# Performance work log

Measured on AMD Instinct MI355X. Metric: run time of the kernel, lower is better.

## Reference

```python
import jax, jax.numpy as jnp
import numpy as np

RES, SKIP, NCLS, K = 256, 512, 256, 2
NUM_LAYERS, NUM_STACKS = 10, 3
NL = NUM_LAYERS * NUM_STACKS
DILATIONS = [2 ** (i % NUM_LAYERS) for i in range(NL)]


def _causal_conv(x, W, b, dilation):
    # x: [B, Cin, T], W: [Cout, Cin, K] -> [B, Cout, T]
    # Original pads both sides by d*(K-1) then slices the right pad off,
    # which is exactly a left-only pad.
    pad = dilation * (W.shape[-1] - 1)
    y = jax.lax.conv_general_dilated(
        x, W, window_strides=(1,), padding=[(pad, 0)],
        rhs_dilation=(dilation,), dimension_numbers=('NCH', 'OIH', 'NCH'))
    return y + b[None, :, None]


def _pw(x, W, b):
    # 1x1 conv: x [B,C,T], W [O,C] -> [B,O,T]
    return jnp.einsum('oc,bct->bot', W, x) + b[None, :, None]


def setup_inputs() -> dict:
    key = jax.random.key(0)
    ks = jax.random.split(key, 16)
    s = 0.05
    return {
        'x': jax.random.normal(ks[0], (4, 1, 8192), dtype=jnp.float32),
        'W_start': jax.random.normal(ks[1], (RES, 1, K), dtype=jnp.float32) * s,
        'b_start': jnp.zeros((RES,), dtype=jnp.float32),
        'Wd': jax.random.normal(ks[2], (NL, RES, RES, K), dtype=jnp.float32) * s,
        'bd': jnp.zeros((NL, RES), dtype=jnp.float32),
        'Wr': jax.random.normal(ks[3], (NL, RES, RES), dtype=jnp.float32) * s,
        'br': jnp.zeros((NL, RES), dtype=jnp.float32),
        'Ws': jax.random.normal(ks[4], (NL, SKIP, RES), dtype=jnp.float32) * s,
        'bs': jnp.zeros((NL, SKIP), dtype=jnp.float32),
        'W_end1': jax.random.normal(ks[5], (SKIP, SKIP), dtype=jnp.float32) * s,
        'b_end1': jnp.zeros((SKIP,), dtype=jnp.float32),
        'W_end2': jax.random.normal(ks[6], (NCLS, SKIP), dtype=jnp.float32) * s,
        'b_end2': jnp.zeros((NCLS,), dtype=jnp.float32),
    }


def reference(x, W_start, b_start, Wd, bd, Wr, br, Ws, bs, W_end1, b_end1, W_end2, b_end2):
    h = _causal_conv(x, W_start, b_start, 1)  # [B, RES, T]
    skip_sum = jnp.zeros((x.shape[0], SKIP, x.shape[2]), dtype=x.dtype)
    for i in range(NL):
        d = _causal_conv(h, Wd[i], bd[i], DILATIONS[i])
        gated = jnp.tanh(d) * jax.nn.sigmoid(d)
        h = h + _pw(gated, Wr[i], br[i])
        skip_sum = skip_sum + _pw(gated, Ws[i], bs[i])
    out = jax.nn.relu(skip_sum)
    out = jax.nn.relu(_pw(out, W_end1, b_end1))
    out = _pw(out, W_end2, b_end2)
    return out[:, :, -1]  # [B, NCLS]
```

## Files before the change

### kernel.cpp

```cpp
#include <hip/hip_runtime.h>

#define BATCH 4
#define T 8192
#define RES 256
#define SKIPC 512
#define NCLSC 256
#define NLAYERS 30
#define T0 5120
#define TBUF 3072
#define NT 32
#define STR 264
#define HFSTR 260
#define GRIDP 384
#define MAXTILES 96

typedef __attribute__((ext_vector_type(8))) short short8x;
typedef __attribute__((ext_vector_type(4))) float floatx4;
typedef unsigned short ushort_t;
typedef unsigned long long ull;

__device__ __forceinline__ ushort_t f2bf(float f) {
    unsigned u = __float_as_uint(f);
    u += 0x7fffu + ((u >> 16) & 1u);
    return (ushort_t)(u >> 16);
}
__device__ __forceinline__ float bf2f(ushort_t h) {
    return __uint_as_float(((unsigned)h) << 16);
}

__device__ __forceinline__ ull cload(const ull* p) {
    return __hip_atomic_load(p, __ATOMIC_RELAXED, __HIP_MEMORY_SCOPE_AGENT);
}
__device__ __forceinline__ void cstore(ull* p, ull v) {
    __hip_atomic_store(p, v, __ATOMIC_RELAXED, __HIP_MEMORY_SCOPE_AGENT);
}

#define WAITF(P) while (__hip_atomic_load((P), __ATOMIC_RELAXED, __HIP_MEMORY_SCOPE_AGENT) == 0) \
                     __builtin_amdgcn_s_sleep(1)

#define MFMA __builtin_amdgcn_mfma_f32_16x16x32_bf16

__global__ __launch_bounds__(256) void prep_kernel(
    const float* __restrict__ Wd, const float* __restrict__ Wr,
    const float* __restrict__ Ws,
    ushort_t* __restrict__ Aswz, ushort_t* __restrict__ Rswz,
    ushort_t* __restrict__ WsT)
{
    long id = (long)blockIdx.x * 256 + threadIdx.x;
    const long R0 = 30L * 131072, R1 = 30L * 65536, R2 = 30L * 131072;
    if (id < R0) {
        long l = id >> 17; int r = (int)(id & 131071);
        int j = r & 7, lane = (r >> 3) & 63, f = (r >> 9) & 1, s = (r >> 10) & 15, wv = r >> 14;
        int row = wv * 32 + f * 16 + (lane & 15);
        int k = s * 32 + (lane >> 4) * 8 + j;
        int cin = k & 255, kk = k >> 8;
        Aswz[id] = f2bf(Wd[((l * 256 + row) * 256 + cin) * 2 + kk]);
        return;
    }
    id -= R0;
    if (id < R1) {
        long l = id >> 16; int r = (int)(id & 65535);
        int j = r & 7, lane = (r >> 3) & 63, f = (r >> 9) & 1, s = (r >> 10) & 7, wv = r >> 13;
        int row = wv * 32 + f * 16 + (lane & 15);
        int k = s * 32 + (lane >> 4) * 8 + j;
        Rswz[id] = f2bf(Wr[(l * 256 + row) * 256 + k]);
        return;
    }
    id -= R1;
    if (id < R2) {
        int o = (int)(id & 511); long rest = id >> 9; int cin = (int)(rest & 255); long l = rest >> 8;
        WsT[id] = f2bf(Ws[(l * 512 + o) * 256 + cin]);
    }
}

__global__ __launch_bounds__(256) void start_kernel(
    const float* __restrict__ x, const float* __restrict__ Wst,
    const float* __restrict__ bst, float* __restrict__ hf, ushort_t* __restrict__ hb)
{
    int id = blockIdx.x * 256 + threadIdx.x;
    int c = id & 255;
    int ti = (id >> 8) % TBUF;
    int b  = (id >> 8) / TBUF;
    int t = T0 + ti;
    float v = Wst[2 * c] * x[b * T + t - 1] + Wst[2 * c + 1] * x[b * T + t] + bst[c];
    hf[id] = v;
    hb[id] = f2bf(v);
}

__global__ __launch_bounds__(512, 2) void fused_layers_kernel(
    const float* __restrict__ hf,
    const ushort_t* __restrict__ hb0,
    const ushort_t* __restrict__ Asw,
    const float* __restrict__ bd,
    const ushort_t* __restrict__ Rsw,
    const float* __restrict__ br,
    float* __restrict__ gstore,
    ushort_t* __restrict__ hbC,
    int* __restrict__ flg)
{
    __shared__ __align__(16) ushort_t hbL[NT * STR];
    __shared__ __align__(16) ushort_t tp[NT * STR];
    __shared__ __align__(16) float hfL[NT * HFSTR];

    const int tid = threadIdx.x;
    const int wv = tid >> 6, lane = tid & 63;
    const int quad = lane >> 4, l16 = lane & 15;
    const int mb = wv * 32;
    const int u0 = l16 * STR + quad * 8;
    const int u1 = u0 + 16 * STR;
    const int B = blockIdx.x;
    const int b = B / MAXTILES, tile = B % MAXTILES;
    const int tb = 8192 - NT * (tile + 1);

    const float* __restrict__ hfg = hf + (size_t)b * TBUF * RES;
    const ushort_t* __restrict__ hbg = hb0 + (size_t)b * TBUF * RES;

    #pragma unroll
    for (int p = 0; p < 4; ++p) {
        int c = p * 512 + tid;
        int row = c >> 6, q = (c & 63) * 4;
        *(float4*)&hfL[row * HFSTR + q] =
            *(const float4*)(hfg + (size_t)(tb - T0 + row) * RES + q);
    }
    #pragma unroll
    for (int p = 0; p < 2; ++p) {
        int c = p * 512 + tid;
        int row = c >> 5, q = (c & 31) * 8;
        *(short8x*)&hbL[row * STR + q] =
            *(const short8x*)(hbg + (size_t)(tb - T0 + row) * RES + q);
    }
    __syncthreads();

    int rem = 3069;
    int ntiles_prev = 0;
    size_t cur_off = 0, prev_off = 0;

    for (int i = 0; i < NLAYERS; ++i) {
        const int dil = 1 << (i % 10);
        rem -= dil;
        const int s_out = 8191 - rem;
        const int ntiles = (1 + rem + 31) >> 5;
        if (tile >= ntiles) break;

        const ushort_t* __restrict__ aw =
            Asw + (size_t)i * (RES * 512) + (size_t)wv * 16384 + lane * 8;
        const ushort_t* __restrict__ rw =
            Rsw + (size_t)i * (RES * RES) + (size_t)wv * 8192 + lane * 8;
        const float* __restrict__ bdL = bd + i * RES;
        const float* __restrict__ brL = br + i * RES;

        const int dil_eff = dil < NT ? dil : NT;
        const int rdelta = dil < NT ? 1 : (dil >> 5);
        const int r = tile + rdelta;
        const bool remote_valid = (i > 0) && (r < ntiles_prev);
        const bool do_stage = (i == 0) || remote_valid;
        const ushort_t* hbCp = nullptr;
        if (remote_valid)
            hbCp = hbC + prev_off + ((size_t)b * ntiles_prev + r) * (size_t)dil_eff * RES;

        const ushort_t* bp0 = ((l16      >= dil_eff) ? &hbL[(l16      - dil) * STR]
                                                     : &tp[l16 * STR]) + quad * 8;
        const ushort_t* bp1 = ((16 + l16 >= dil_eff) ? &hbL[(16 + l16 - dil) * STR]
                                                     : &tp[(16 + l16) * STR]) + quad * 8;

        floatx4 acc00, acc01, acc10, acc11;
        {
            float4 c0 = *(const float4*)(bdL + mb + quad * 4);
            float4 c1 = *(const float4*)(bdL + mb + 16 + quad * 4);
            acc00 = acc01 = (floatx4){c0.x, c0.y, c0.z, c0.w};
            acc10 = acc11 = (floatx4){c1.x, c1.y, c1.z, c1.w};
        }

        #define LD(BASE, S, OFF) (*(const short8x*)((BASE) + (S) * 1024 + (OFF)))

        {
            short8x a0 = LD(aw, 8, 0), a1 = LD(aw, 8, 512);
            #pragma unroll
            for (int s = 0; s < 8; ++s) {
                short8x n0 = a0, n1 = a1;
                if (s < 7) { n0 = LD(aw, 9 + s, 0); n1 = LD(aw, 9 + s, 512); }
                const int ko = s * 32;
                short8x g0 = *(const short8x*)&hbL[ko + u0];
                short8x g1 = *(const short8x*)&hbL[ko + u1];
                acc00 = MFMA(a0, g0, acc00, 0, 0, 0);
                acc10 = MFMA(a1, g0, acc10, 0, 0, 0);
                acc01 = MFMA(a0, g1, acc01, 0, 0, 0);
                acc11 = MFMA(a1, g1, acc11, 0, 0, 0);
                a0 = n0; a1 = n1;
            }
        }

        if (do_stage) {
            if (i > 0) { WAITF(flg + ((i - 1) * BATCH + b) * MAXTILES + r); }
            if (i == 0) {
                #pragma unroll
                for (int p = 0; p < 2; ++p) {
                    int c = p * 512 + tid;
                    int row = c >> 5, q = (c & 31) * 8;
                    if (row < dil_eff) {
                        int tt = tb + row - dil;
                        tt = tt < T0 ? T0 : tt;
                        *(short8x*)&tp[row * STR + q] =
                            *(const short8x*)(hbg + (size_t)(tt - T0) * RES + q);
                    }
                }
            } else {
                #pragma unroll
                for (int p = 0; p < 2; ++p) {
                    int c = p * 512 + tid;
                    int row = c >> 5, q = (c & 31) * 8;
                    if (row < dil_eff) {
                        const ull* src = (const ull*)(hbCp + (size_t)row * RES + q);
                        ull v0 = cload(src), v1 = cload(src + 1);
                        ull* dst = (ull*)&tp[row * STR + q];
                        dst[0] = v0; dst[1] = v1;
                    }
                }
            }
            __syncthreads();
        }

        {
            short8x a0 = LD(aw, 0, 0), a1 = LD(aw, 0, 512);
            #pragma unroll
            for (int s = 0; s < 8; ++s) {
                short8x n0 = a0, n1 = a1;
                if (s < 7) { n0 = LD(aw, 1 + s, 0); n1 = LD(aw, 1 + s, 512); }
                const int ko = s * 32;
                short8x g0 = *(const short8x*)(bp0 + ko);
                short8x g1 = *(const short8x*)(bp1 + ko);
                acc00 = MFMA(a0, g0, acc00, 0, 0, 0);
                acc10 = MFMA(a1, g0, acc10, 0, 0, 0);
                acc01 = MFMA(a0, g1, acc01, 0, 0, 0);
                acc11 = MFMA(a1, g1, acc11, 0, 0, 0);
                a0 = n0; a1 = n1;
            }
        }

        short8x ra0 = LD(rw, 0, 0), ra1 = LD(rw, 0, 512);
        __syncthreads();

        #define GATE(ACC, MF, NF) do {                                             \
            float gf[4]; ull pk = 0;                                               \
            _Pragma("unroll")                                                      \
            for (int rr = 0; rr < 4; ++rr) {                                       \
                float d = fmaxf((ACC)[rr], -30.f);                                 \
                float u = __expf(-d);                                              \
                gf[rr] = (1.f - u) * __builtin_amdgcn_rcpf(1.f + u * u);           \
                pk |= ((ull)f2bf(gf[rr])) << (16 * rr);                            \
            }                                                                      \
            const int n = (NF) * 16 + l16;                                         \
            const int m = mb + (MF) * 16 + quad * 4;                               \
            *(ull*)&tp[n * STR + m] = pk;                                          \
            if (tile == 0 && n == 31) {                                            \
                float4 g4 = {gf[0], gf[1], gf[2], gf[3]};                          \
                *(float4*)&gstore[((size_t)i * BATCH + b) * RES + m] = g4;         \
            }                                                                      \
        } while (0)
        GATE(acc00, 0, 0); GATE(acc01, 0, 1); GATE(acc10, 1, 0); GATE(acc11, 1, 1);
        #undef GATE
        __syncthreads();

        floatx4 r00, r01, r10, r11;
        {
            float4 c0 = *(const float4*)(brL + mb + quad * 4);
            float4 c1 = *(const float4*)(brL + mb + 16 + quad * 4);
            r00 = r01 = (floatx4){c0.x, c0.y, c0.z, c0.w};
            r10 = r11 = (floatx4){c1.x, c1.y, c1.z, c1.w};
        }
        {
            short8x a0 = ra0, a1 = ra1;
            #pragma unroll
            for (int s = 0; s < 8; ++s) {
                short8x n0 = a0, n1 = a1;
                if (s < 7) { n0 = LD(rw, 1 + s, 0); n1 = LD(rw, 1 + s, 512); }
                const int ko = s * 32;
                short8x g0 = *(const short8x*)&tp[ko + u0];
                short8x g1 = *(const short8x*)&tp[ko + u1];
                r00 = MFMA(a0, g0, r00, 0, 0, 0);
                r10 = MFMA(a1, g0, r10, 0, 0, 0);
                r01 = MFMA(a0, g1, r01, 0, 0, 0);
                r11 = MFMA(a1, g1, r11, 0, 0, 0);
                a0 = n0; a1 = n1;
            }
        }
        #undef LD

        const int dnext = (i < NLAYERS - 1) ? (1 << ((i + 1) % 10)) : 0;
        const int Ci = dnext < NT ? dnext : NT;
        const int rdn = (dnext < NT) ? 1 : (dnext >> 5);
        const bool wrC = (Ci > 0) && (tile >= rdn);
        const int pubrow = NT - Ci;
        ushort_t* hbCc = hbC + cur_off + ((size_t)b * ntiles + tile) * (size_t)Ci * RES;

        #define EPI(NF, RA, RB) do {                                               \
            const int n = (NF) * 16 + l16;                                         \
            if (tb + n >= s_out) {                                                 \
                const int m0 = mb + quad * 4;                                      \
                {                                                                  \
                    float4 ho = *(const float4*)&hfL[n * HFSTR + m0];              \
                    float4 hn = {ho.x + (RA)[0], ho.y + (RA)[1],                   \
                                 ho.z + (RA)[2], ho.w + (RA)[3]};                  \
                    *(float4*)&hfL[n * HFSTR + m0] = hn;                           \
                    ull pk = (ull)f2bf(hn.x) | ((ull)f2bf(hn.y) << 16)             \
                           | ((ull)f2bf(hn.z) << 32) | ((ull)f2bf(hn.w) << 48);    \
                    *(ull*)&hbL[n * STR + m0] = pk;                                \
                    if (wrC && n >= pubrow)                                        \
                        cstore((ull*)(hbCc + (size_t)(n - pubrow) * RES + m0), pk);\
                }                                                                  \
                {                                                                  \
                    const int m1 = m0 + 16;                                        \
                    float4 ho = *(const float4*)&hfL[n * HFSTR + m1];              \
                    float4 hn = {ho.x + (RB)[0], ho.y + (RB)[1],                   \
                                 ho.z + (RB)[2], ho.w + (RB)[3]};                  \
                    *(float4*)&hfL[n * HFSTR + m1] = hn;                           \
                    ull pk = (ull)f2bf(hn.x) | ((ull)f2bf(hn.y) << 16)             \
                           | ((ull)f2bf(hn.z) << 32) | ((ull)f2bf(hn.w) << 48);    \
                    *(ull*)&hbL[n * STR + m1] = pk;                                \
                    if (wrC && n >= pubrow)                                        \
                        cstore((ull*)(hbCc + (size_t)(n - pubrow) * RES + m1), pk);\
                }                                                                  \
            }                                                                      \
        } while (0)
        EPI(0, r00, r10);
        EPI(1, r01, r11);
        #undef EPI

        asm volatile("s_waitcnt vmcnt(0)" ::: "memory");
        __syncthreads();
        if (tid == 0)
            __hip_atomic_store(flg + ((size_t)i * BATCH + b) * MAXTILES + tile, 1,
                               __ATOMIC_RELAXED, __HIP_MEMORY_SCOPE_AGENT);

        ntiles_prev = ntiles;
        prev_off = cur_off;
        cur_off += (size_t)BATCH * ntiles * Ci * RES;
    }
}

__global__ __launch_bounds__(512) void skip_kernel(
    const ushort_t* __restrict__ WsT, const float* __restrict__ bs,
    const float* __restrict__ gstore, float* __restrict__ skip)
{
    const int l = blockIdx.x, b = blockIdx.y, o = threadIdx.x;
    const ushort_t* w = WsT + (size_t)l * 131072;
    const float* g = gstore + (size_t)(l * BATCH + b) * RES;
    float a = bs[l * SKIPC + o];
    #pragma unroll 4
    for (int cin = 0; cin < RES; ++cin)
        a = fmaf(bf2f(w[cin * SKIPC + o]), g[cin], a);
    atomicAdd(&skip[b * SKIPC + o], a);
}

__global__ __launch_bounds__(256) void end1_kernel(
    const float* __restrict__ skip, const float* __restrict__ W1,
    const float* __restrict__ b1, float* __restrict__ e1ws)
{
    __shared__ float s[SKIPC];
    __shared__ float part[256];
    const int b = blockIdx.x, og = blockIdx.y, tid = threadIdx.x;
    s[tid]       = fmaxf(skip[b * SKIPC + tid], 0.f);
    s[tid + 256] = fmaxf(skip[b * SKIPC + tid + 256], 0.f);
    __syncthreads();
    const int o_l = tid >> 3, kp = tid & 7;
    const int o = og * 32 + o_l;
    const float* w = W1 + (size_t)o * SKIPC + kp * 64;
    const float* sp = s + kp * 64;
    float a = 0.f;
    #pragma unroll 8
    for (int j = 0; j < 64; ++j) a = fmaf(w[j], sp[j], a);
    part[tid] = a;
    __syncthreads();
    if (tid < 32) {
        float r = b1[og * 32 + tid];
        #pragma unroll
        for (int k = 0; k < 8; ++k) r += part[tid * 8 + k];
        e1ws[b * SKIPC + og * 32 + tid] = fmaxf(r, 0.f);
    }
}

__global__ __launch_bounds__(256) void end2_kernel(
    const float* __restrict__ e1ws, const float* __restrict__ W2,
    const float* __restrict__ b2, float* __restrict__ out)
{
    __shared__ float e[SKIPC];
    __shared__ float part[256];
    const int b = blockIdx.x, og = blockIdx.y, tid = threadIdx.x;
    e[tid]       = e1ws[b * SKIPC + tid];
    e[tid + 256] = e1ws[b * SKIPC + tid + 256];
    __syncthreads();
    const int o_l = tid >> 3, kp = tid & 7;
    const int cls = og * 32 + o_l;
    const float* w = W2 + (size_t)cls * SKIPC + kp * 64;
    const float* ep = e + kp * 64;
    float a = 0.f;
    #pragma unroll 8
    for (int j = 0; j < 64; ++j) a = fmaf(w[j], ep[j], a);
    part[tid] = a;
    __syncthreads();
    if (tid < 32) {
        float r = b2[og * 32 + tid];
        #pragma unroll
        for (int k = 0; k < 8; ++k) r += part[tid * 8 + k];
        out[b * NCLSC + og * 32 + tid] = r;
    }
}

extern "C" void kernel_launch(void* const* d_in, const int* in_sizes, int n_in,
                              void* d_out, int out_size, void* d_ws, size_t ws_size,
                              hipStream_t stream)
{
    const float* x   = (const float*)d_in[0];
    const float* Wst = (const float*)d_in[1];
    const float* bst = (const float*)d_in[2];
    const float* Wd  = (const float*)d_in[3];
    const float* bd  = (const float*)d_in[4];
    const float* Wr  = (const float*)d_in[5];
    const float* br  = (const float*)d_in[6];
    const float* Ws  = (const float*)d_in[7];
    const float* bs  = (const float*)d_in[8];
    const float* W1  = (const float*)d_in[9];
    const float* b1  = (const float*)d_in[10];
    const float* W2  = (const float*)d_in[11];
    const float* b2  = (const float*)d_in[12];
    float* out = (float*)d_out;

    size_t hbC_shorts = 0;
    {
        int rem = 3069;
        for (int i = 0; i < NLAYERS; ++i) {
            int d = 1 << (i % 10);
            rem -= d;
            int ntl = (1 + rem + 31) >> 5;
            int dn = (i < NLAYERS - 1) ? (1 << ((i + 1) % 10)) : 0;
            int Ci = (dn < NT) ? dn : NT;
            hbC_shorts += (size_t)BATCH * ntl * Ci * RES;
        }
    }

    char* w = (char*)d_ws;
    float* hf     = (float*)w;     w += (size_t)BATCH * TBUF * RES * 4;
    ushort_t* hb0 = (ushort_t*)w;  w += (size_t)BATCH * TBUF * RES * 2;
    ushort_t* Asw = (ushort_t*)w;  w += (size_t)NLAYERS * RES * 512 * 2;
    ushort_t* Rsw = (ushort_t*)w;  w += (size_t)NLAYERS * RES * RES * 2;
    ushort_t* WsT = (ushort_t*)w;  w += (size_t)NLAYERS * RES * SKIPC * 2;
    float* gstore = (float*)w;     w += (size_t)NLAYERS * BATCH * RES * 4;
    float* skip   = (float*)w;     w += (size_t)BATCH * SKIPC * 4;
    float* e1ws   = (float*)w;     w += (size_t)BATCH * SKIPC * 4;
    ushort_t* hbC = (ushort_t*)w;  w += hbC_shorts * 2;
    int* flg      = (int*)w;       w += (size_t)NLAYERS * BATCH * MAXTILES * 4;

    prep_kernel<<<38400, 256, 0, stream>>>(Wd, Wr, Ws, Asw, Rsw, WsT);
    start_kernel<<<(BATCH * TBUF * RES) / 256, 256, 0, stream>>>(x, Wst, bst, hf, hb0);
    hipMemsetAsync(skip, 0, BATCH * SKIPC * 4, stream);
    hipMemsetAsync(flg, 0, (size_t)NLAYERS * BATCH * MAXTILES * 4, stream);

    fused_layers_kernel<<<GRIDP, 512, 0, stream>>>(
        hf, hb0, Asw, bd, Rsw, br, gstore, hbC, flg);

    skip_kernel<<<dim3(NLAYERS, BATCH), 512, 0, stream>>>(WsT, bs, gstore, skip);
    end1_kernel<<<dim3(BATCH, 16), 256, 0, stream>>>(skip, W1, b1, e1ws);
    end2_kernel<<<dim3(BATCH, 8), 256, 0, stream>>>(e1ws, W2, b2, out);
}
```

Measured before the change: 420.0 us.

## Vectorize weight prep kernels and software-pipeline MFMA weight loads across phases

Splits the scalar per-element weight conversion kernel into a vectorized Wd/Wr swizzle kernel and a shared-memory transpose kernel for Ws, so prep reads float4 and writes packed 64-bit bf16 groups. In the fused layer kernel, the per-step prefetch loops are replaced by a register double-buffer (q/p banks) with sched barriers. Weight loads for the next phase, and for the next layer's first dilated-conv chunk, are issued before the current MFMAs. This is meant to hide global weight-load latency behind MFMA work and across the wait/stage sync, at the cost of many more live vector registers under the 512-thread, 2-block launch bound.

```diff
diff --git a/kernel.cpp b/kernel.cpp
--- a/kernel.cpp
+++ b/kernel.cpp
@@ -39,37 +39,77 @@
                      __builtin_amdgcn_s_sleep(1)
 
 #define MFMA __builtin_amdgcn_mfma_f32_16x16x32_bf16
-
-__global__ __launch_bounds__(256) void prep_kernel(
+#define SB() __builtin_amdgcn_sched_barrier(0)
+
+__global__ __launch_bounds__(512) void prep_ar_kernel(
     const float* __restrict__ Wd, const float* __restrict__ Wr,
-    const float* __restrict__ Ws,
-    ushort_t* __restrict__ Aswz, ushort_t* __restrict__ Rswz,
-    ushort_t* __restrict__ WsT)
-{
-    long id = (long)blockIdx.x * 256 + threadIdx.x;
-    const long R0 = 30L * 131072, R1 = 30L * 65536, R2 = 30L * 131072;
-    if (id < R0) {
-        long l = id >> 17; int r = (int)(id & 131071);
-        int j = r & 7, lane = (r >> 3) & 63, f = (r >> 9) & 1, s = (r >> 10) & 15, wv = r >> 14;
+    ushort_t* __restrict__ Aswz, ushort_t* __restrict__ Rswz)
+{
+    int id = blockIdx.x * 512 + threadIdx.x;
+    const int NA = 245760;
+    if (id < NA) {
+        int lane = id & 63, f = (id >> 6) & 1, s = (id >> 7) & 7, wv = (id >> 10) & 7;
+        int l = id >> 13;
         int row = wv * 32 + f * 16 + (lane & 15);
-        int k = s * 32 + (lane >> 4) * 8 + j;
-        int cin = k & 255, kk = k >> 8;
-        Aswz[id] = f2bf(Wd[((l * 256 + row) * 256 + cin) * 2 + kk]);
+        int cinb = s * 32 + (lane >> 4) * 8;
+        const float4* p = (const float4*)(Wd + (((size_t)l * 256 + row) * 256 + cinb) * 2);
+        float4 a = p[0], b = p[1], c = p[2], d = p[3];
+        ull e0 = (ull)f2bf(a.x) | ((ull)f2bf(a.z) << 16) | ((ull)f2bf(b.x) << 32) | ((ull)f2bf(b.z) << 48);
+        ull e1 = (ull)f2bf(c.x) | ((ull)f2bf(c.z) << 16) | ((ull)f2bf(d.x) << 32) | ((ull)f2bf(d.z) << 48);
+        ull o0 = (ull)f2bf(a.y) | ((ull)f2bf(a.w) << 16) | ((ull)f2bf(b.y) << 32) | ((ull)f2bf(b.w) << 48);
+        ull o1 = (ull)f2bf(c.y) | ((ull)f2bf(c.w) << 16) | ((ull)f2bf(d.y) << 32) | ((ull)f2bf(d.w) << 48);
+        ull* outE = (ull*)(Aswz + ((size_t)((((l * 8 + wv) * 16 + s) * 2 + f) * 64 + lane)) * 8);
+        ull* outO = (ull*)(Aswz + ((size_t)((((l * 8 + wv) * 16 + s + 8) * 2 + f) * 64 + lane)) * 8);
+        outE[0] = e0; outE[1] = e1;
+        outO[0] = o0; outO[1] = o1;
         return;
     }
-    id -= R0;
-    if (id < R1) {
-        long l = id >> 16; int r = (int)(id & 65535);
-        int j = r & 7, lane = (r >> 3) & 63, f = (r >> 9) & 1, s = (r >> 10) & 7, wv = r >> 13;
+    id -= NA;
+    {
+        int lane = id & 63, f = (id >> 6) & 1, s = (id >> 7) & 7, wv = (id >> 10) & 7;
+        int l = id >> 13;
         int row = wv * 32 + f * 16 + (lane & 15);
-        int k = s * 32 + (lane >> 4) * 8 + j;
-        Rswz[id] = f2bf(Wr[(l * 256 + row) * 256 + k]);
-        return;
-    }
-    id -= R1;
-    if (id < R2) {
-        int o = (int)(id & 511); long rest = id >> 9; int cin = (int)(rest & 255); long l = rest >> 8;
-        WsT[id] = f2bf(Ws[(l * 512 + o) * 256 + cin]);
+        int kb = s * 32 + (lane >> 4) * 8;
+        const float4* p = (const float4*)(Wr + ((size_t)l * 256 + row) * 256 + kb);
+        float4 a = p[0], b = p[1];
+        ull v0 = (ull)f2bf(a.x) | ((ull)f2bf(a.y) << 16) | ((ull)f2bf(a.z) << 32) | ((ull)f2bf(a.w) << 48);
+        ull v1 = (ull)f2bf(b.x) | ((ull)f2bf(b.y) << 16) | ((ull)f2bf(b.z) << 32) | ((ull)f2bf(b.w) << 48);
+        ull* outp = (ull*)(Rswz + ((size_t)((((l * 8 + wv) * 8 + s) * 2 + f) * 64 + lane)) * 8);
+        outp[0] = v0; outp[1] = v1;
+    }
+}
+
+__global__ __launch_bounds__(256) void prep_w_kernel(
+    const float* __restrict__ Ws, ushort_t* __restrict__ WsT)
+{
+    __shared__ float t[64][65];
+    const int bi = blockIdx.x;
+    const int l = bi >> 5;
+    const int ob = (bi & 31) >> 2, cb = bi & 3;
+    const int tid = threadIdx.x;
+    const int o_l = tid >> 2, part = tid & 3;
+    const float* src = Ws + ((size_t)l * 512 + ob * 64 + o_l) * 256 + cb * 64 + part * 16;
+    #pragma unroll
+    for (int u = 0; u < 4; ++u) {
+        float4 v = ((const float4*)src)[u];
+        t[o_l][part * 16 + u * 4 + 0] = v.x;
+        t[o_l][part * 16 + u * 4 + 1] = v.y;
+        t[o_l][part * 16 + u * 4 + 2] = v.z;
+        t[o_l][part * 16 + u * 4 + 3] = v.w;
+    }
+    __syncthreads();
+    const int cin_l = tid >> 2;
+    #pragma unroll
+    for (int w = 0; w < 2; ++w) {
+        int ow8 = (tid & 3) + w * 4;
+        float x0 = t[ow8 * 8 + 0][cin_l], x1 = t[ow8 * 8 + 1][cin_l];
+        float x2 = t[ow8 * 8 + 2][cin_l], x3 = t[ow8 * 8 + 3][cin_l];
+        float x4 = t[ow8 * 8 + 4][cin_l], x5 = t[ow8 * 8 + 5][cin_l];
+        float x6 = t[ow8 * 8 + 6][cin_l], x7 = t[ow8 * 8 + 7][cin_l];
+        ull u0 = (ull)f2bf(x0) | ((ull)f2bf(x1) << 16) | ((ull)f2bf(x2) << 32) | ((ull)f2bf(x3) << 48);
+        ull u1 = (ull)f2bf(x4) | ((ull)f2bf(x5) << 16) | ((ull)f2bf(x6) << 32) | ((ull)f2bf(x7) << 48);
+        ull* outp = (ull*)(WsT + ((size_t)l * 256 + cb * 64 + cin_l) * 512 + ob * 64 + ow8 * 8);
+        outp[0] = u0; outp[1] = u1;
     }
 }
 
@@ -129,6 +169,18 @@
         *(short8x*)&hbL[row * STR + q] =
             *(const short8x*)(hbg + (size_t)(tb - T0 + row) * RES + q);
     }
+
+    #define LD(BASE, S, OFF) (*(const short8x*)((BASE) + (S) * 1024 + (OFF)))
+
+    short8x q0a, q0b, q1a, q1b, q2a, q2b, q3a, q3b;
+    short8x p0a, p0b, p1a, p1b, p2a, p2b, p3a, p3b;
+    {
+        const ushort_t* aw0 = Asw + (size_t)wv * 16384 + lane * 8;
+        q0a = LD(aw0, 8, 0);  q0b = LD(aw0, 8, 512);
+        q1a = LD(aw0, 9, 0);  q1b = LD(aw0, 9, 512);
+        q2a = LD(aw0, 10, 0); q2b = LD(aw0, 10, 512);
+        q3a = LD(aw0, 11, 0); q3b = LD(aw0, 11, 512);
+    }
     __syncthreads();
 
     int rem = 3069;
@@ -171,24 +223,37 @@
             acc10 = acc11 = (floatx4){c1.x, c1.y, c1.z, c1.w};
         }
 
-        #define LD(BASE, S, OFF) (*(const short8x*)((BASE) + (S) * 1024 + (OFF)))
-
-        {
-            short8x a0 = LD(aw, 8, 0), a1 = LD(aw, 8, 512);
-            #pragma unroll
-            for (int s = 0; s < 8; ++s) {
-                short8x n0 = a0, n1 = a1;
-                if (s < 7) { n0 = LD(aw, 9 + s, 0); n1 = LD(aw, 9 + s, 512); }
-                const int ko = s * 32;
-                short8x g0 = *(const short8x*)&hbL[ko + u0];
-                short8x g1 = *(const short8x*)&hbL[ko + u1];
-                acc00 = MFMA(a0, g0, acc00, 0, 0, 0);
-                acc10 = MFMA(a1, g0, acc10, 0, 0, 0);
-                acc01 = MFMA(a0, g1, acc01, 0, 0, 0);
-                acc11 = MFMA(a1, g1, acc11, 0, 0, 0);
-                a0 = n0; a1 = n1;
-            }
-        }
+        #define CVH(A0_, A1_, KO) do {                                             \
+            short8x g0 = *(const short8x*)&hbL[(KO) + u0];                         \
+            short8x g1 = *(const short8x*)&hbL[(KO) + u1];                         \
+            acc00 = MFMA(A0_, g0, acc00, 0, 0, 0);                                 \
+            acc10 = MFMA(A1_, g0, acc10, 0, 0, 0);                                 \
+            acc01 = MFMA(A0_, g1, acc01, 0, 0, 0);                                 \
+            acc11 = MFMA(A1_, g1, acc11, 0, 0, 0);                                 \
+        } while (0)
+        #define CVB(A0_, A1_, KO) do {                                             \
+            short8x g0 = *(const short8x*)(bp0 + (KO));                            \
+            short8x g1 = *(const short8x*)(bp1 + (KO));                            \
+            acc00 = MFMA(A0_, g0, acc00, 0, 0, 0);                                 \
+            acc10 = MFMA(A1_, g0, acc10, 0, 0, 0);                                 \
+            acc01 = MFMA(A0_, g1, acc01, 0, 0, 0);                                 \
+            acc11 = MFMA(A1_, g1, acc11, 0, 0, 0);                                 \
+        } while (0)
+
+        p0a = LD(aw, 12, 0); p0b = LD(aw, 12, 512);
+        p1a = LD(aw, 13, 0); p1b = LD(aw, 13, 512);
+        p2a = LD(aw, 14, 0); p2b = LD(aw, 14, 512);
+        p3a = LD(aw, 15, 0); p3b = LD(aw, 15, 512);
+        SB();
+        CVH(q0a, q0b, 0); CVH(q1a, q1b, 32); CVH(q2a, q2b, 64); CVH(q3a, q3b, 96);
+        SB();
+        q0a = LD(aw, 0, 0); q0b = LD(aw, 0, 512);
+        q1a = LD(aw, 1, 0); q1b = LD(aw, 1, 512);
+        q2a = LD(aw, 2, 0); q2b = LD(aw, 2, 512);
+        q3a = LD(aw, 3, 0); q3b = LD(aw, 3, 512);
+        SB();
+        CVH(p0a, p0b, 128); CVH(p1a, p1b, 160); CVH(p2a, p2b, 192); CVH(p3a, p3b, 224);
+        SB();
 
         if (do_stage) {
             if (i > 0) { WAITF(flg + ((i - 1) * BATCH + b) * MAXTILES + r); }
@@ -220,24 +285,27 @@
             __syncthreads();
         }
 
-        {
-            short8x a0 = LD(aw, 0, 0), a1 = LD(aw, 0, 512);
-            #pragma unroll
-            for (int s = 0; s < 8; ++s) {
-                short8x n0 = a0, n1 = a1;
-                if (s < 7) { n0 = LD(aw, 1 + s, 0); n1 = LD(aw, 1 + s, 512); }
-                const int ko = s * 32;
-                short8x g0 = *(const short8x*)(bp0 + ko);
-                short8x g1 = *(const short8x*)(bp1 + ko);
-                acc00 = MFMA(a0, g0, acc00, 0, 0, 0);
-                acc10 = MFMA(a1, g0, acc10, 0, 0, 0);
-                acc01 = MFMA(a0, g1, acc01, 0, 0, 0);
-                acc11 = MFMA(a1, g1, acc11, 0, 0, 0);
-                a0 = n0; a1 = n1;
-            }
-        }
-
-        short8x ra0 = LD(rw, 0, 0), ra1 = LD(rw, 0, 512);
+        p0a = LD(aw, 4, 0); p0b = LD(aw, 4, 512);
+        p1a = LD(aw, 5, 0); p1b = LD(aw, 5, 512);
+        p2a = LD(aw, 6, 0); p2b = LD(aw, 6, 512);
+        p3a = LD(aw, 7, 0); p3b = LD(aw, 7, 512);
+        SB();
+        CVB(q0a, q0b, 0); CVB(q1a, q1b, 32); CVB(q2a, q2b, 64); CVB(q3a, q3b, 96);
+        SB();
+        q0a = LD(rw, 0, 0); q0b = LD(rw, 0, 512);
+        q1a = LD(rw, 1, 0); q1b = LD(rw, 1, 512);
+        q2a = LD(rw, 2, 0); q2b = LD(rw, 2, 512);
+        q3a = LD(rw, 3, 0); q3b = LD(rw, 3, 512);
+        SB();
+        CVB(p0a, p0b, 128); CVB(p1a, p1b, 160); CVB(p2a, p2b, 192); CVB(p3a, p3b, 224);
+        SB();
+        p0a = LD(rw, 4, 0); p0b = LD(rw, 4, 512);
+        p1a = LD(rw, 5, 0); p1b = LD(rw, 5, 512);
+        p2a = LD(rw, 6, 0); p2b = LD(rw, 6, 512);
+        p3a = LD(rw, 7, 0); p3b = LD(rw, 7, 512);
+        SB();
+        #undef CVH
+        #undef CVB
         __syncthreads();
 
         #define GATE(ACC, MF, NF) do {                                             \
@@ -268,23 +336,26 @@
             r00 = r01 = (floatx4){c0.x, c0.y, c0.z, c0.w};
             r10 = r11 = (floatx4){c1.x, c1.y, c1.z, c1.w};
         }
-        {
-            short8x a0 = ra0, a1 = ra1;
-            #pragma unroll
-            for (int s = 0; s < 8; ++s) {
-                short8x n0 = a0, n1 = a1;
-                if (s < 7) { n0 = LD(rw, 1 + s, 0); n1 = LD(rw, 1 + s, 512); }
-                const int ko = s * 32;
-                short8x g0 = *(const short8x*)&tp[ko + u0];
-                short8x g1 = *(const short8x*)&tp[ko + u1];
-                r00 = MFMA(a0, g0, r00, 0, 0, 0);
-                r10 = MFMA(a1, g0, r10, 0, 0, 0);
-                r01 = MFMA(a0, g1, r01, 0, 0, 0);
-                r11 = MFMA(a1, g1, r11, 0, 0, 0);
-                a0 = n0; a1 = n1;
-            }
+        #define RVV(A0_, A1_, KO) do {                                             \
+            short8x g0 = *(const short8x*)&tp[(KO) + u0];                          \
+            short8x g1 = *(const short8x*)&tp[(KO) + u1];                          \
+            r00 = MFMA(A0_, g0, r00, 0, 0, 0);                                     \
+            r10 = MFMA(A1_, g0, r10, 0, 0, 0);                                     \
+            r01 = MFMA(A0_, g1, r01, 0, 0, 0);                                     \
+            r11 = MFMA(A1_, g1, r11, 0, 0, 0);                                     \
+        } while (0)
+        RVV(q0a, q0b, 0); RVV(q1a, q1b, 32); RVV(q2a, q2b, 64); RVV(q3a, q3b, 96);
+        SB();
+        if (i < NLAYERS - 1) {
+            const ushort_t* awn = aw + RES * 512;
+            q0a = LD(awn, 8, 0);  q0b = LD(awn, 8, 512);
+            q1a = LD(awn, 9, 0);  q1b = LD(awn, 9, 512);
+            q2a = LD(awn, 10, 0); q2b = LD(awn, 10, 512);
+            q3a = LD(awn, 11, 0); q3b = LD(awn, 11, 512);
         }
-        #undef LD
+        SB();
+        RVV(p0a, p0b, 128); RVV(p1a, p1b, 160); RVV(p2a, p2b, 192); RVV(p3a, p3b, 224);
+        #undef RVV
 
         const int dnext = (i < NLAYERS - 1) ? (1 << ((i + 1) % 10)) : 0;
         const int Ci = dnext < NT ? dnext : NT;
@@ -336,6 +407,7 @@
         prev_off = cur_off;
         cur_off += (size_t)BATCH * ntiles * Ci * RES;
     }
+    #undef LD
 }
 
 __global__ __launch_bounds__(512) void skip_kernel(
@@ -450,7 +522,8 @@
     ushort_t* hbC = (ushort_t*)w;  w += hbC_shorts * 2;
     int* flg      = (int*)w;       w += (size_t)NLAYERS * BATCH * MAXTILES * 4;
 
-    prep_kernel<<<38400, 256, 0, stream>>>(Wd, Wr, Ws, Asw, Rsw, WsT);
+    prep_ar_kernel<<<960, 512, 0, stream>>>(Wd, Wr, Asw, Rsw);
+    prep_w_kernel<<<960, 256, 0, stream>>>(Ws, WsT);
     start_kernel<<<(BATCH * TBUF * RES) / 256, 256, 0, stream>>>(x, Wst, bst, hf, hb0);
     hipMemsetAsync(skip, 0, BATCH * SKIPC * 4, stream);
     hipMemsetAsync(flg, 0, (size_t)NLAYERS * BATCH * MAXTILES * 4, stream);
```

New measurement: 445.5 us. 1.06x slower.
